# Kernel tuning notes

Hardware: AMD Instinct MI355X
Metric: run time of the kernel (lower is better)

The kernel has to match this reference:

```python
import jax, jax.numpy as jnp
import numpy as np

N = 100000
E = 1200000
D = 64
EPS = 1e-5  # BatchNorm1d default eps


def setup_inputs() -> dict:
    key = jax.random.key(0)
    ks = jax.random.split(key, 5)
    x = jax.random.normal(ks[0], (N, D), dtype=jnp.float32)
    edge_index = jax.random.randint(ks[1], (2, E), 0, N, dtype=jnp.int32)
    W1 = jax.random.normal(ks[2], (D, D), dtype=jnp.float32) * (1.0 / np.sqrt(D))
    W2 = jax.random.normal(ks[3], (D, D), dtype=jnp.float32) * (1.0 / np.sqrt(D))
    return {
        'x': x,
        'edge_index': edge_index,
        'W1': W1,
        'b1': jnp.zeros((D,), jnp.float32),
        'gamma1': jnp.ones((D,), jnp.float32),
        'beta1': jnp.zeros((D,), jnp.float32),
        'W2': W2,
        'b2': jnp.zeros((D,), jnp.float32),
        'gamma2': jnp.ones((D,), jnp.float32),
        'beta2': jnp.zeros((D,), jnp.float32),
    }


def gcn_conv(x, src, dst, W, b):
    # GCNConv: xw = x @ W; add self-loops; symmetric deg^{-1/2} normalization;
    # scatter-add aggregation over incoming edges; + bias.
    xw = x @ W  # [N, out]
    # degree including self-loop (edge weight 1)
    deg = jnp.zeros((x.shape[0],), x.dtype).at[dst].add(1.0) + 1.0  # [N]
    dinv = jax.lax.rsqrt(deg)
    norm = dinv[src] * dinv[dst]  # [E]
    agg = jnp.zeros_like(xw).at[dst].add(norm[:, None] * xw[src])
    agg = agg + (dinv * dinv)[:, None] * xw  # self-loop term: deg^{-1} * xw
    return agg + b


def batchnorm(x, gamma, beta):
    # training-mode BatchNorm1d over node dimension (biased variance)
    mu = x.mean(axis=0)
    var = x.var(axis=0)
    return gamma * (x - mu) * jax.lax.rsqrt(var + EPS) + beta


def reference(x, edge_index, W1, b1, gamma1, beta1, W2, b2, gamma2, beta2):
    src, dst = edge_index[0], edge_index[1]
    h = gcn_conv(x, src, dst, W1, b1)
    h = jax.nn.leaky_relu(batchnorm(h, gamma1, beta1), 0.01)
    # dropout p=0.0 -> identity
    h = gcn_conv(h, src, dst, W2, b2)
    h = jax.nn.leaky_relu(batchnorm(h, gamma2, beta2), 0.01)
    return h
```

## Files before the change

kernel.cpp:

```cpp
#include <hip/hip_runtime.h>
#include <hip/hip_bf16.h>

#define NN 100000
#define NE 1200000
#define DD 64
#define EPS 1e-5f

#define NB 196
#define GEMM_BLOCKS (NN / 32)
#define HIST_BLOCKS 256
#define PART_BLOCKS 256
#define EPH ((NE + HIST_BLOCKS - 1) / HIST_BLOCKS)
#define EPB ((NE + PART_BLOCKS - 1) / PART_BLOCKS)

template <bool BN>
__device__ __forceinline__ void gemm_tile(const float* __restrict__ X,
                                          const float* __restrict__ W,
                                          __hip_bfloat16* __restrict__ XWh,
                                          const float* __restrict__ stats,
                                          const float* __restrict__ gamma,
                                          const float* __restrict__ beta,
                                          int blk) {
    __shared__ float xs[32][64];
    __shared__ float sc_s[64], sh_s[64];
    int col = threadIdx.x & 63;
    int rg  = threadIdx.x >> 6;
    int row0 = blk * 32;

    if (BN) {
        if (threadIdx.x < 64) {
            const float inv_n = 1.0f / (float)NN;
            float mu  = stats[threadIdx.x] * inv_n;
            float var = stats[64 + threadIdx.x] * inv_n - mu * mu;
            float sc  = gamma[threadIdx.x] * rsqrtf(var + EPS);
            sc_s[threadIdx.x] = sc;
            sh_s[threadIdx.x] = beta[threadIdx.x] - sc * mu;
        }
        __syncthreads();
    }

    float w[64];
#pragma unroll
    for (int k = 0; k < 64; ++k) w[k] = W[k * 64 + col];

    for (int i = threadIdx.x; i < 32 * 16; i += 256) {
        int r = i >> 4, c4 = i & 15;
        float4 v = ((const float4*)(X + (size_t)(row0 + r) * 64))[c4];
        if (BN) {
            float4 s4 = ((const float4*)sc_s)[c4];
            float4 h4 = ((const float4*)sh_s)[c4];
            v.x = s4.x * v.x + h4.x; v.x = fmaxf(v.x, 0.01f * v.x);
            v.y = s4.y * v.y + h4.y; v.y = fmaxf(v.y, 0.01f * v.y);
            v.z = s4.z * v.z + h4.z; v.z = fmaxf(v.z, 0.01f * v.z);
            v.w = s4.w * v.w + h4.w; v.w = fmaxf(v.w, 0.01f * v.w);
        }
        ((float4*)&xs[r][0])[c4] = v;
    }
    __syncthreads();

    float acc[8];
#pragma unroll
    for (int r8 = 0; r8 < 8; ++r8) {
        int r = rg * 8 + r8;
        float a = 0.0f;
#pragma unroll
        for (int k = 0; k < 64; k += 4) {
            float4 xv = *((const float4*)&xs[r][k]);
            a += xv.x * w[k] + xv.y * w[k + 1] + xv.z * w[k + 2] + xv.w * w[k + 3];
        }
        acc[r8] = a;
    }
#pragma unroll
    for (int r8 = 0; r8 < 8; ++r8)
        XWh[(size_t)(row0 + rg * 8 + r8) * 64 + col] = __float2bfloat16(acc[r8]);
}

__global__ __launch_bounds__(256) void k_histscan(const int* __restrict__ dst,
                                                  int* __restrict__ cnt196,
                                                  int* __restrict__ done,
                                                  int* __restrict__ bo,
                                                  int* __restrict__ cur) {
    __shared__ int h[NB];
    __shared__ int s[256];
    __shared__ int lastflag;
    for (int t = threadIdx.x; t < NB; t += 256) h[t] = 0;
    __syncthreads();
    int s0 = blockIdx.x * EPH;
    int s1 = s0 + EPH; if (s1 > NE) s1 = NE;
    for (int i = s0 + threadIdx.x; i < s1; i += 256)
        atomicAdd(&h[dst[i] >> 9], 1);
    __syncthreads();
    for (int t = threadIdx.x; t < NB; t += 256)
        if (h[t]) atomicAdd(&cnt196[t], h[t]);
    __threadfence();
    if (threadIdx.x == 0)
        lastflag = (atomicAdd(done, 1) == HIST_BLOCKS - 1);
    __syncthreads();
    if (lastflag) {
        int t = threadIdx.x;
        int v = (t < NB) ? atomicAdd(&cnt196[t], 0) : 0;
        s[t] = v;
        __syncthreads();
        for (int o = 1; o < 256; o <<= 1) {
            int u = (t >= o) ? s[t - o] : 0;
            __syncthreads();
            s[t] += u;
            __syncthreads();
        }
        if (t < NB) {
            int ex = s[t] - v;
            bo[t] = ex;
            cur[t] = ex;
        }
        if (t == 0) bo[NB] = NE;
    }
}

__global__ __launch_bounds__(256) void k_pg(const float* __restrict__ X,
                                            const float* __restrict__ W,
                                            __hip_bfloat16* __restrict__ XWh,
                                            const int* __restrict__ src,
                                            const int* __restrict__ dst,
                                            int* __restrict__ cur,
                                            int* __restrict__ ebuf) {
    if (blockIdx.x < PART_BLOCKS) {
        __shared__ int h[NB];
        for (int t = threadIdx.x; t < NB; t += 256) h[t] = 0;
        __syncthreads();
        int s0 = blockIdx.x * EPB;
        int s1 = s0 + EPB; if (s1 > NE) s1 = NE;
        for (int i = s0 + threadIdx.x; i < s1; i += 256)
            atomicAdd(&h[dst[i] >> 9], 1);
        __syncthreads();
        for (int t = threadIdx.x; t < NB; t += 256) {
            int c = h[t];
            h[t] = c ? atomicAdd(&cur[t], c) : 0;
        }
        __syncthreads();
        for (int i = s0 + threadIdx.x; i < s1; i += 256) {
            int d = dst[i];
            int p = atomicAdd(&h[d >> 9], 1);
            ebuf[p] = src[i] | ((d & 511) << 17);
        }
    } else {
        gemm_tile<false>(X, W, XWh, nullptr, nullptr, nullptr,
                         (int)blockIdx.x - PART_BLOCKS);
    }
}

__global__ __launch_bounds__(256) void k_gemm2(const float* __restrict__ X,
                                               const float* __restrict__ W,
                                               __hip_bfloat16* __restrict__ XWh,
                                               const float* __restrict__ stats,
                                               const float* __restrict__ gamma,
                                               const float* __restrict__ beta) {
    gemm_tile<true>(X, W, XWh, stats, gamma, beta, blockIdx.x);
}

__global__ __launch_bounds__(512) void k_bucket(const int* __restrict__ ebuf,
                                                const int* __restrict__ bo,
                                                int* __restrict__ off,
                                                float* __restrict__ dinv,
                                                int* __restrict__ esrc) {
    __shared__ int s[512];
    int b = blockIdx.x, t = threadIdx.x;
    int base = b << 9;
    int e0 = bo[b], e1 = bo[b + 1];
    s[t] = 0;
    __syncthreads();
    for (int e = e0 + t; e < e1; e += 512)
        atomicAdd(&s[ebuf[e] >> 17], 1);
    __syncthreads();
    int deg = s[t];
    if (base + t < NN) dinv[base + t] = rsqrtf((float)deg + 1.0f);
    for (int o = 1; o < 512; o <<= 1) {
        int u = (t >= o) ? s[t - o] : 0;
        __syncthreads();
        s[t] += u;
        __syncthreads();
    }
    int gstart = e0 + s[t] - deg;
    if (base + t < NN) off[base + t] = gstart;
    if (b == NB - 1 && t == 0) off[NN] = NE;
    __syncthreads();
    s[t] = gstart;
    __syncthreads();
    for (int e = e0 + t; e < e1; e += 512) {
        int v = ebuf[e];
        int p = atomicAdd(&s[v >> 17], 1);
        esrc[p] = v & 0x1FFFF;
    }
}

__device__ __forceinline__ void bf16x8(uint4 u, float* f) {
    f[0] = __uint_as_float(u.x << 16);
    f[1] = __uint_as_float(u.x & 0xFFFF0000u);
    f[2] = __uint_as_float(u.y << 16);
    f[3] = __uint_as_float(u.y & 0xFFFF0000u);
    f[4] = __uint_as_float(u.z << 16);
    f[5] = __uint_as_float(u.z & 0xFFFF0000u);
    f[6] = __uint_as_float(u.w << 16);
    f[7] = __uint_as_float(u.w & 0xFFFF0000u);
}

__global__ __launch_bounds__(256) void k_agg(const __hip_bfloat16* __restrict__ XWh,
                                             const int* __restrict__ off,
                                             const int* __restrict__ esrc,
                                             const float* __restrict__ dinv,
                                             float* __restrict__ out) {
    const uint4* __restrict__ XW4 = (const uint4*)XWh;
    int team = threadIdx.x >> 3;
    int sub  = threadIdx.x & 7;
    int node = blockIdx.x * 32 + team;

    float di = dinv[node];
    float a[8], b[8], r0[8], r1[8];
    uint4 us = XW4[(size_t)node * 8 + sub];
    bf16x8(us, a);
#pragma unroll
    for (int i = 0; i < 8; ++i) { a[i] *= di; b[i] = 0.0f; }

    int e0 = off[node], e1 = off[node + 1];
    int e = e0;
    for (; e + 1 < e1; e += 2) {
        int s0 = esrc[e];
        int s1 = esrc[e + 1];
        float n0 = dinv[s0], n1 = dinv[s1];
        uint4 u0 = XW4[(size_t)s0 * 8 + sub];
        uint4 u1 = XW4[(size_t)s1 * 8 + sub];
        bf16x8(u0, r0);
        bf16x8(u1, r1);
#pragma unroll
        for (int i = 0; i < 8; ++i) a[i] += n0 * r0[i];
#pragma unroll
        for (int i = 0; i < 8; ++i) b[i] += n1 * r1[i];
    }
    if (e < e1) {
        int s0 = esrc[e];
        float n0 = dinv[s0];
        uint4 u0 = XW4[(size_t)s0 * 8 + sub];
        bf16x8(u0, r0);
#pragma unroll
        for (int i = 0; i < 8; ++i) a[i] += n0 * r0[i];
    }
#pragma unroll
    for (int i = 0; i < 8; ++i) a[i] = (a[i] + b[i]) * di;

    float4* o4 = (float4*)out;
    o4[(size_t)node * 16 + sub * 2]     = make_float4(a[0], a[1], a[2], a[3]);
    o4[(size_t)node * 16 + sub * 2 + 1] = make_float4(a[4], a[5], a[6], a[7]);
}

__global__ __launch_bounds__(256) void k_stats(const float* __restrict__ X,
                                               float* __restrict__ stats, int n) {
    __shared__ float ls[4][64], lq[4][64];
    int lane = threadIdx.x & 63, rg = threadIdx.x >> 6;
    float s = 0.0f, sq = 0.0f;
    for (int r = blockIdx.x * 4 + rg; r < n; r += gridDim.x * 4) {
        float v = X[(size_t)r * 64 + lane];
        s += v; sq += v * v;
    }
    ls[rg][lane] = s; lq[rg][lane] = sq;
    __syncthreads();
    if (rg == 0) {
        s  = ls[0][lane] + ls[1][lane] + ls[2][lane] + ls[3][lane];
        sq = lq[0][lane] + lq[1][lane] + lq[2][lane] + lq[3][lane];
        atomicAdd(&stats[lane], s);
        atomicAdd(&stats[64 + lane], sq);
    }
}

__global__ __launch_bounds__(256) void k_bnact(const float* __restrict__ X,
                                               float* __restrict__ Y,
                                               const float* __restrict__ stats,
                                               const float* __restrict__ gamma,
                                               const float* __restrict__ beta,
                                               int n) {
    int lane = threadIdx.x & 63, rg = threadIdx.x >> 6;
    float inv_n = 1.0f / (float)n;
    float mu  = stats[lane] * inv_n;
    float var = stats[64 + lane] * inv_n - mu * mu;
    float sc  = gamma[lane] * rsqrtf(var + EPS);
    float sh  = beta[lane] - sc * mu;
    for (int r = blockIdx.x * 4 + rg; r < n; r += gridDim.x * 4) {
        float v = X[(size_t)r * 64 + lane];
        v = sc * v + sh;
        Y[(size_t)r * 64 + lane] = fmaxf(v, 0.01f * v);
    }
}

extern "C" void kernel_launch(void* const* d_in, const int* in_sizes, int n_in,
                              void* d_out, int out_size, void* d_ws, size_t ws_size,
                              hipStream_t stream) {
    const float* x   = (const float*)d_in[0];
    const int*   ei  = (const int*)d_in[1];
    const int*   src = ei;
    const int*   dst = ei + NE;
    const float* W1  = (const float*)d_in[2];
    const float* g1  = (const float*)d_in[4];
    const float* be1 = (const float*)d_in[5];
    const float* W2  = (const float*)d_in[6];
    const float* g2  = (const float*)d_in[8];
    const float* be2 = (const float*)d_in[9];
    float* out = (float*)d_out;

    char* ws = (char*)d_ws;
    size_t p = 0;
    auto alloc = [&](size_t bytes) {
        size_t o = p;
        p = (p + bytes + 255) & ~(size_t)255;
        return o;
    };
    int*   zeroed  = (int*)(ws + alloc(2304));
    int*   cnt196  = zeroed;
    float* stats   = (float*)(zeroed + 256);
    int*   done    = zeroed + 512;
    int*   bo      = (int*)(ws + alloc((size_t)(NB + 1) * 4));
    int*   cur     = (int*)(ws + alloc((size_t)NB * 4));
    int*   ebuf    = (int*)(ws + alloc((size_t)NE * 4));
    int*   esrc    = (int*)(ws + alloc((size_t)NE * 4));
    int*   off     = (int*)(ws + alloc((size_t)(NN + 1) * 4));
    float* dinv    = (float*)(ws + alloc((size_t)NN * 4));
    __hip_bfloat16* Ah = (__hip_bfloat16*)(ws + alloc((size_t)NN * DD * 2));
    float* B       = (float*)(ws + alloc((size_t)NN * DD * 4));
    (void)ws_size; (void)in_sizes; (void)n_in; (void)out_size;

    hipMemsetAsync(zeroed, 0, 2304, stream);

    k_histscan<<<HIST_BLOCKS, 256, 0, stream>>>(dst, cnt196, done, bo, cur);
    k_pg<<<PART_BLOCKS + GEMM_BLOCKS, 256, 0, stream>>>(x, W1, Ah, src, dst, cur, ebuf);
    k_bucket<<<NB, 512, 0, stream>>>(ebuf, bo, off, dinv, esrc);

    k_agg<<<NN / 32, 256, 0, stream>>>(Ah, off, esrc, dinv, B);
    k_stats<<<512, 256, 0, stream>>>(B, stats, NN);

    k_gemm2<<<GEMM_BLOCKS, 256, 0, stream>>>(B, W2, Ah, stats, g1, be1);
    k_agg<<<NN / 32, 256, 0, stream>>>(Ah, off, esrc, dinv, B);
    k_stats<<<512, 256, 0, stream>>>(B, stats + 128, NN);
    k_bnact<<<1024, 256, 0, stream>>>(B, out, stats + 128, g2, be2, NN);
}
```

Measured before the change: 290.3 us.

## Use bf16 MFMA with hi/lo split for the dense GEMM tile

The scalar FP32 X@W tile is replaced with MFMA 16x16x32 bf16 instructions. The activations are split into hi and lo bf16 parts so accuracy stays near FP32, and W is transposed into shared memory as bf16. Tiles grow to 64 rows with bounds checks, so there are half as many blocks. Each block re-converts W and the output stores are scattered 2-byte writes, and W itself is rounded to bf16, which loses some precision.

```diff
diff --git a/kernel.cpp b/kernel.cpp
--- a/kernel.cpp
+++ b/kernel.cpp
@@ -7,11 +7,22 @@
 #define EPS 1e-5f
 
 #define NB 196
-#define GEMM_BLOCKS (NN / 32)
+#define GEMM_BLOCKS ((NN + 63) / 64)
 #define HIST_BLOCKS 256
 #define PART_BLOCKS 256
 #define EPH ((NE + HIST_BLOCKS - 1) / HIST_BLOCKS)
 #define EPB ((NE + PART_BLOCKS - 1) / PART_BLOCKS)
+
+typedef short bf16x8_t __attribute__((ext_vector_type(8)));
+typedef float f32x4_t  __attribute__((ext_vector_type(4)));
+
+__device__ __forceinline__ short f2bf(float f) {
+    __hip_bfloat16 h = __float2bfloat16(f);
+    return reinterpret_cast<short&>(h);
+}
+__device__ __forceinline__ float bf2f(short s) {
+    return __uint_as_float(((unsigned)(unsigned short)s) << 16);
+}
 
 template <bool BN>
 __device__ __forceinline__ void gemm_tile(const float* __restrict__ X,
@@ -21,31 +32,36 @@
                                           const float* __restrict__ gamma,
                                           const float* __restrict__ beta,
                                           int blk) {
-    __shared__ float xs[32][64];
+    __shared__ __align__(16) short xhi[64 * 72];
+    __shared__ __align__(16) short xlo[64 * 72];
+    __shared__ __align__(16) short wt[64 * 72];
     __shared__ float sc_s[64], sh_s[64];
-    int col = threadIdx.x & 63;
-    int rg  = threadIdx.x >> 6;
-    int row0 = blk * 32;
+    int t = threadIdx.x;
+    int row0 = blk * 64;
 
     if (BN) {
-        if (threadIdx.x < 64) {
+        if (t < 64) {
             const float inv_n = 1.0f / (float)NN;
-            float mu  = stats[threadIdx.x] * inv_n;
-            float var = stats[64 + threadIdx.x] * inv_n - mu * mu;
-            float sc  = gamma[threadIdx.x] * rsqrtf(var + EPS);
-            sc_s[threadIdx.x] = sc;
-            sh_s[threadIdx.x] = beta[threadIdx.x] - sc * mu;
-        }
-        __syncthreads();
-    }
-
-    float w[64];
-#pragma unroll
-    for (int k = 0; k < 64; ++k) w[k] = W[k * 64 + col];
-
-    for (int i = threadIdx.x; i < 32 * 16; i += 256) {
+            float mu  = stats[t] * inv_n;
+            float var = stats[64 + t] * inv_n - mu * mu;
+            float sc  = gamma[t] * rsqrtf(var + EPS);
+            sc_s[t] = sc;
+            sh_s[t] = beta[t] - sc * mu;
+        }
+        __syncthreads();
+    }
+
+    for (int i = t; i < 64 * 64; i += 256) {
+        int k = i >> 6, n = i & 63;
+        wt[n * 72 + k] = f2bf(W[k * 64 + n]);
+    }
+
+    for (int it = 0; it < 4; ++it) {
+        int i = it * 256 + t;
         int r = i >> 4, c4 = i & 15;
-        float4 v = ((const float4*)(X + (size_t)(row0 + r) * 64))[c4];
+        int grow = row0 + r;
+        float4 v = make_float4(0.f, 0.f, 0.f, 0.f);
+        if (grow < NN) v = ((const float4*)(X + (size_t)grow * 64))[c4];
         if (BN) {
             float4 s4 = ((const float4*)sc_s)[c4];
             float4 h4 = ((const float4*)sh_s)[c4];
@@ -54,25 +70,50 @@
             v.z = s4.z * v.z + h4.z; v.z = fmaxf(v.z, 0.01f * v.z);
             v.w = s4.w * v.w + h4.w; v.w = fmaxf(v.w, 0.01f * v.w);
         }
-        ((float4*)&xs[r][0])[c4] = v;
-    }
-    __syncthreads();
-
-    float acc[8];
-#pragma unroll
-    for (int r8 = 0; r8 < 8; ++r8) {
-        int r = rg * 8 + r8;
-        float a = 0.0f;
-#pragma unroll
-        for (int k = 0; k < 64; k += 4) {
-            float4 xv = *((const float4*)&xs[r][k]);
-            a += xv.x * w[k] + xv.y * w[k + 1] + xv.z * w[k + 2] + xv.w * w[k + 3];
-        }
-        acc[r8] = a;
-    }
-#pragma unroll
-    for (int r8 = 0; r8 < 8; ++r8)
-        XWh[(size_t)(row0 + rg * 8 + r8) * 64 + col] = __float2bfloat16(acc[r8]);
+        short h0 = f2bf(v.x), h1 = f2bf(v.y), h2 = f2bf(v.z), h3 = f2bf(v.w);
+        short l0 = f2bf(v.x - bf2f(h0)), l1 = f2bf(v.y - bf2f(h1));
+        short l2 = f2bf(v.z - bf2f(h2)), l3 = f2bf(v.w - bf2f(h3));
+        int base = r * 72 + c4 * 4;
+        *(short4*)&xhi[base] = make_short4(h0, h1, h2, h3);
+        *(short4*)&xlo[base] = make_short4(l0, l1, l2, l3);
+    }
+    __syncthreads();
+
+    int w = t >> 6;
+    int l = t & 63;
+    int fr = l & 15;
+    int fq = l >> 4;
+    int abase = (w * 16 + fr) * 72 + fq * 8;
+
+    bf16x8_t ahi0 = *(const bf16x8_t*)&xhi[abase];
+    bf16x8_t ahi1 = *(const bf16x8_t*)&xhi[abase + 32];
+    bf16x8_t alo0 = *(const bf16x8_t*)&xlo[abase];
+    bf16x8_t alo1 = *(const bf16x8_t*)&xlo[abase + 32];
+
+    f32x4_t acc[4];
+#pragma unroll
+    for (int c = 0; c < 4; ++c) acc[c] = (f32x4_t){0.f, 0.f, 0.f, 0.f};
+
+#pragma unroll
+    for (int c = 0; c < 4; ++c) {
+        int bbase = (c * 16 + fr) * 72 + fq * 8;
+        bf16x8_t b0 = *(const bf16x8_t*)&wt[bbase];
+        bf16x8_t b1 = *(const bf16x8_t*)&wt[bbase + 32];
+        acc[c] = __builtin_amdgcn_mfma_f32_16x16x32_bf16(ahi0, b0, acc[c], 0, 0, 0);
+        acc[c] = __builtin_amdgcn_mfma_f32_16x16x32_bf16(alo0, b0, acc[c], 0, 0, 0);
+        acc[c] = __builtin_amdgcn_mfma_f32_16x16x32_bf16(ahi1, b1, acc[c], 0, 0, 0);
+        acc[c] = __builtin_amdgcn_mfma_f32_16x16x32_bf16(alo1, b1, acc[c], 0, 0, 0);
+    }
+
+#pragma unroll
+    for (int c = 0; c < 4; ++c) {
+#pragma unroll
+        for (int i = 0; i < 4; ++i) {
+            int grow = row0 + w * 16 + fq * 4 + i;
+            if (grow < NN)
+                XWh[(size_t)grow * 64 + c * 16 + fr] = __float2bfloat16(acc[c][i]);
+        }
+    }
 }
 
 __global__ __launch_bounds__(256) void k_histscan(const int* __restrict__ dst,
@@ -192,7 +233,7 @@
     }
 }
 
-__device__ __forceinline__ void bf16x8(uint4 u, float* f) {
+__device__ __forceinline__ void bf16x8d(uint4 u, float* f) {
     f[0] = __uint_as_float(u.x << 16);
     f[1] = __uint_as_float(u.x & 0xFFFF0000u);
     f[2] = __uint_as_float(u.y << 16);
@@ -216,7 +257,7 @@
     float di = dinv[node];
     float a[8], b[8], r0[8], r1[8];
     uint4 us = XW4[(size_t)node * 8 + sub];
-    bf16x8(us, a);
+    bf16x8d(us, a);
 #pragma unroll
     for (int i = 0; i < 8; ++i) { a[i] *= di; b[i] = 0.0f; }
 
@@ -228,8 +269,8 @@
         float n0 = dinv[s0], n1 = dinv[s1];
         uint4 u0 = XW4[(size_t)s0 * 8 + sub];
         uint4 u1 = XW4[(size_t)s1 * 8 + sub];
-        bf16x8(u0, r0);
-        bf16x8(u1, r1);
+        bf16x8d(u0, r0);
+        bf16x8d(u1, r1);
 #pragma unroll
         for (int i = 0; i < 8; ++i) a[i] += n0 * r0[i];
 #pragma unroll
@@ -239,7 +280,7 @@
         int s0 = esrc[e];
         float n0 = dinv[s0];
         uint4 u0 = XW4[(size_t)s0 * 8 + sub];
-        bf16x8(u0, r0);
+        bf16x8d(u0, r0);
 #pragma unroll
         for (int i = 0; i < 8; ++i) a[i] += n0 * r0[i];
     }
```

Result: faster. 280.4 us (-3.4%).
